# Performance work log

Measured on AMD Instinct MI355X. Metric: run time of the kernel, lower is better.

The kernel has to match this reference:

```python
import jax, jax.numpy as jnp
import numpy as np

B, S, D, H, F = 64, 512, 1024, 1024, 1024  # note: module requires H == D
EPS = 1e-6


def setup_inputs() -> dict:
    key = jax.random.key(0)
    ks = jax.random.split(key, 14)
    p = lambda k, shape: 0.02 * jax.random.normal(k, shape, dtype=jnp.float32)
    return {
        "hidden_state": jax.random.normal(ks[0], (B, S, D), dtype=jnp.float32),
        "field_hidden_state": jax.random.normal(ks[1], (B, S, F), dtype=jnp.float32),
        "input": jax.random.normal(ks[2], (B, D), dtype=jnp.float32),
        "finished": jnp.zeros((B, 1), dtype=bool),
        "W1": p(ks[3], (H, D)), "b1": p(ks[4], (H,)),
        "W2": p(ks[5], (H, D)), "b2": p(ks[6], (H,)),
        "W3": p(ks[7], (H, 2 * D)), "b3": p(ks[8], (H,)),
        "W4": p(ks[9], (H, F)), "b4": p(ks[10], (H,)),
        "W5": p(ks[11], (H, D)), "b5": p(ks[12], (H,)),
    }


def _norm_over_seq(w):
    # manual exp/max/sum softmax over seq dim (axis 0) with 1e-6 guard, as in torch
    w = jnp.exp(w - jnp.max(w, axis=0, keepdims=True))
    return w / (EPS + jnp.sum(w, axis=0, keepdims=True))


def reference(hidden_state, field_hidden_state, input, finished,
              W1, b1, W2, b2, W3, b3, W4, b4, W5, b5):
    hs = jnp.transpose(hidden_state, (1, 0, 2))        # [S, B, D]
    fs = jnp.transpose(field_hidden_state, (1, 0, 2))  # [S, B, F]
    phi_h = jnp.tanh(hs @ W1.T + b1)                   # [S, B, H]
    phi_f = jnp.tanh(fs @ W4.T + b4)                   # [S, B, H]

    gamma_h = jnp.tanh(input @ W2.T + b2)              # [B, H]
    weights = _norm_over_seq(jnp.sum(phi_h * gamma_h, axis=2, keepdims=True))  # [S, B, 1]

    alpha_h = jnp.tanh(input @ W5.T + b5)              # [B, H]
    field_w = _norm_over_seq(jnp.sum(phi_f * alpha_h, axis=2, keepdims=True))  # [S, B, 1]

    wf = weights * field_w
    weights = wf / (EPS + jnp.sum(wf, axis=0, keepdims=True))  # [S, B, 1]

    context = jnp.sum(hs * weights, axis=0)            # [B, D]
    out = jnp.concatenate([context, input], axis=-1) @ W3.T + b3  # [B, H]
    out = jnp.where(finished, jnp.zeros_like(out), out)
    return out, weights
```

## Files before the change

### kernel.cpp

```cpp
#include <hip/hip_runtime.h>

#define EPS 1e-6f

typedef _Float16 f16;
typedef _Float16 f16x8 __attribute__((ext_vector_type(8)));
typedef _Float16 f16x4 __attribute__((ext_vector_type(4)));
typedef float f32x4 __attribute__((ext_vector_type(4)));

__device__ __forceinline__ float tanh_fast(float x) {
    float e = __expf(2.0f * x);
    return 1.0f - 2.0f / (e + 1.0f);
}

__global__ __launch_bounds__(256) void wconv_kernel(
    const float* __restrict__ W1, const float* __restrict__ W4,
    f16* __restrict__ W1h, f16* __restrict__ W4h)
{
    int gid = blockIdx.x * 256 + threadIdx.x;
    const float4* s1 = (const float4*)W1;
    const float4* s4 = (const float4*)W4;
    f16x4* d1 = (f16x4*)W1h;
    f16x4* d4 = (f16x4*)W4h;
    #pragma unroll
    for (int r = 0; r < 2; ++r) {
        int i = gid + r * 131072;
        float4 v = s1[i];
        f16x4 o; o[0]=(f16)v.x; o[1]=(f16)v.y; o[2]=(f16)v.z; o[3]=(f16)v.w;
        d1[i] = o;
        float4 u = s4[i];
        f16x4 p; p[0]=(f16)u.x; p[1]=(f16)u.y; p[2]=(f16)u.z; p[3]=(f16)u.w;
        d4[i] = p;
    }
}

__global__ __launch_bounds__(256) void gamal_kernel(
    const float* __restrict__ inp,
    const float* __restrict__ W2, const float* __restrict__ b2,
    const float* __restrict__ W5, const float* __restrict__ b5,
    float* __restrict__ gamm, float* __restrict__ alph)
{
    const float* W  = blockIdx.y ? W5 : W2;
    const float* bs = blockIdx.y ? b5 : b2;
    float* dst      = blockIdx.y ? alph : gamm;
    int wid = threadIdx.x >> 6, lane = threadIdx.x & 63;
    int p = blockIdx.x * 4 + wid;
    int b = p >> 10, h = p & 1023;
    const float4* wr = (const float4*)(W + (size_t)h * 1024);
    const float4* xr = (const float4*)(inp + (size_t)b * 1024);
    float acc = 0.f;
    #pragma unroll
    for (int j = 0; j < 4; ++j) {
        float4 w4 = wr[lane + 64 * j];
        float4 x4 = xr[lane + 64 * j];
        acc += w4.x * x4.x + w4.y * x4.y + w4.z * x4.z + w4.w * x4.w;
    }
    #pragma unroll
    for (int o = 32; o; o >>= 1) acc += __shfl_xor(acc, o);
    if (lane == 0) dst[p] = tanh_fast(acc + bs[h]);
}

__global__ __launch_bounds__(256, 2) void fused_logits_kernel(
    const float* __restrict__ Ahid, const float* __restrict__ Afld,
    const f16* __restrict__ W1h, const f16* __restrict__ W4h,
    const float* __restrict__ b1, const float* __restrict__ b4,
    const float* __restrict__ gamm, const float* __restrict__ alph,
    float* __restrict__ Lh, float* __restrict__ Lf)
{
    const int mat = blockIdx.y;
    const float* A  = mat ? Afld : Ahid;
    const f16* W    = mat ? W4h : W1h;
    const float* bv = mat ? b4 : b1;
    const float* gv = mat ? alph : gamm;
    float* Lg       = mat ? Lf : Lh;

    const int m0 = blockIdx.x << 7;
    const int bidx = m0 >> 9;
    const int t = threadIdx.x;
    const int lane = t & 63;
    const int wid = t >> 6;
    const int wr = wid >> 1, wc = wid & 1;

    __shared__ __align__(16) f16 aL[2][128 * 40];
    __shared__ __align__(16) f16 wL[2][256 * 40];
    __shared__ float rowpart[128][2];

    if (t < 128) { rowpart[t][0] = 0.0f; rowpart[t][1] = 0.0f; }

    const int arow = t >> 1, ahalf = t & 1;
    const float* aG = A + (size_t)(m0 + arow) * 1024 + ahalf * 16;
    f16* aD0 = &aL[0][arow * 40 + ahalf * 16];
    f16* aD1 = &aL[1][arow * 40 + ahalf * 16];
    f16* wD0 = &wL[0][t * 40];
    f16* wD1 = &wL[1][t * 40];

    const int c16 = lane & 15;
    const int rq = lane >> 4;
    const int ks = rq << 3;
    const int rbase = (wr << 6) + c16;
    const int wbase = (wc << 7) + c16;

    f32x4 acc[4][8];

    for (int nc = 0; nc < 4; ++nc) {
        const f16* wG = W + (size_t)((nc << 8) + t) * 1024;
        f32x4 zz = {0.f, 0.f, 0.f, 0.f};
        #pragma unroll
        for (int mi = 0; mi < 4; ++mi)
            #pragma unroll
            for (int ni = 0; ni < 8; ++ni) acc[mi][ni] = zz;

        auto stage = [&](int kk, int buf) {
            const float4* ap = (const float4*)(aG + kk * 32);
            float4 x0 = ap[0], x1 = ap[1], x2 = ap[2], x3 = ap[3];
            const f16x8* wp = (const f16x8*)(wG + kk * 32);
            f16x8 w0 = wp[0], w1 = wp[1], w2 = wp[2], w3 = wp[3];
            f16x8 p0, p1;
            p0[0]=(f16)x0.x; p0[1]=(f16)x0.y; p0[2]=(f16)x0.z; p0[3]=(f16)x0.w;
            p0[4]=(f16)x1.x; p0[5]=(f16)x1.y; p0[6]=(f16)x1.z; p0[7]=(f16)x1.w;
            p1[0]=(f16)x2.x; p1[1]=(f16)x2.y; p1[2]=(f16)x2.z; p1[3]=(f16)x2.w;
            p1[4]=(f16)x3.x; p1[5]=(f16)x3.y; p1[6]=(f16)x3.z; p1[7]=(f16)x3.w;
            f16* ad = buf ? aD1 : aD0;
            f16* wd = buf ? wD1 : wD0;
            *(f16x8*)(ad)      = p0;
            *(f16x8*)(ad + 8)  = p1;
            *(f16x8*)(wd)      = w0;
            *(f16x8*)(wd + 8)  = w1;
            *(f16x8*)(wd + 16) = w2;
            *(f16x8*)(wd + 24) = w3;
        };

        stage(0, 0);
        __syncthreads();

        for (int kk = 0; kk < 32; ++kk) {
            const int cur = kk & 1;
            if (kk < 31) stage(kk + 1, cur ^ 1);
            const f16* aB = aL[cur];
            const f16* wB = wL[cur];
            f16x8 af[4];
            #pragma unroll
            for (int mi = 0; mi < 4; ++mi)
                af[mi] = *(const f16x8*)&aB[(rbase + mi * 16) * 40 + ks];
            #pragma unroll
            for (int ni = 0; ni < 8; ++ni) {
                f16x8 bf = *(const f16x8*)&wB[(wbase + ni * 16) * 40 + ks];
                #pragma unroll
                for (int mi = 0; mi < 4; ++mi)
                    acc[mi][ni] = __builtin_amdgcn_mfma_f32_16x16x32_f16(af[mi], bf, acc[mi][ni], 0, 0, 0);
            }
            __syncthreads();
        }

        float g[8], bb[8];
        #pragma unroll
        for (int ni = 0; ni < 8; ++ni) {
            int h = (nc << 8) + (wc << 7) + ni * 16 + c16;
            g[ni]  = gv[(bidx << 10) + h];
            bb[ni] = bv[h];
        }
        #pragma unroll
        for (int mi = 0; mi < 4; ++mi) {
            float v0 = 0.f, v1 = 0.f, v2 = 0.f, v3 = 0.f;
            #pragma unroll
            for (int ni = 0; ni < 8; ++ni) {
                v0 += tanh_fast(acc[mi][ni][0] + bb[ni]) * g[ni];
                v1 += tanh_fast(acc[mi][ni][1] + bb[ni]) * g[ni];
                v2 += tanh_fast(acc[mi][ni][2] + bb[ni]) * g[ni];
                v3 += tanh_fast(acc[mi][ni][3] + bb[ni]) * g[ni];
            }
            #pragma unroll
            for (int off = 1; off < 16; off <<= 1) {
                v0 += __shfl_xor(v0, off);
                v1 += __shfl_xor(v1, off);
                v2 += __shfl_xor(v2, off);
                v3 += __shfl_xor(v3, off);
            }
            if (c16 == 0) {
                int rb = (wr << 6) + mi * 16 + (rq << 2);
                rowpart[rb + 0][wc] += v0;
                rowpart[rb + 1][wc] += v1;
                rowpart[rb + 2][wc] += v2;
                rowpart[rb + 3][wc] += v3;
            }
        }
    }
    __syncthreads();
    if (t < 128) Lg[m0 + t] = rowpart[t][0] + rowpart[t][1];
}

__device__ __forceinline__ float blockMax(float v, float* sm) {
    #pragma unroll
    for (int o = 32; o; o >>= 1) v = fmaxf(v, __shfl_xor(v, o));
    if ((threadIdx.x & 63) == 0) sm[threadIdx.x >> 6] = v;
    __syncthreads();
    v = fmaxf(fmaxf(sm[0], sm[1]), fmaxf(sm[2], sm[3]));
    __syncthreads();
    return v;
}
__device__ __forceinline__ float blockSum(float v, float* sm) {
    #pragma unroll
    for (int o = 32; o; o >>= 1) v += __shfl_xor(v, o);
    if ((threadIdx.x & 63) == 0) sm[threadIdx.x >> 6] = v;
    __syncthreads();
    v = sm[0] + sm[1] + sm[2] + sm[3];
    __syncthreads();
    return v;
}

__global__ __launch_bounds__(256) void softmax_combine_kernel(
    const float* __restrict__ Lh, const float* __restrict__ Lf,
    float* __restrict__ wfin, float* __restrict__ dout)
{
    __shared__ float sm[4];
    int b = blockIdx.x, t = threadIdx.x;
    float h0 = Lh[b * 512 + t], h1 = Lh[b * 512 + 256 + t];
    float f0 = Lf[b * 512 + t], f1 = Lf[b * 512 + 256 + t];
    float mh = blockMax(fmaxf(h0, h1), sm);
    float mf = blockMax(fmaxf(f0, f1), sm);
    float e0 = __expf(h0 - mh), e1 = __expf(h1 - mh);
    float q0 = __expf(f0 - mf), q1 = __expf(f1 - mf);
    float sh = blockSum(e0 + e1, sm);
    float sf = blockSum(q0 + q1, sm);
    float wh0 = e0 / (EPS + sh), wh1 = e1 / (EPS + sh);
    float wq0 = q0 / (EPS + sf), wq1 = q1 / (EPS + sf);
    float c0 = wh0 * wq0, c1 = wh1 * wq1;
    float sc = blockSum(c0 + c1, sm);
    float r0 = c0 / (EPS + sc), r1 = c1 / (EPS + sc);
    wfin[b * 512 + t]       = r0;
    wfin[b * 512 + 256 + t] = r1;
    dout[65536 + t * 64 + b]         = r0;
    dout[65536 + (256 + t) * 64 + b] = r1;
}

__global__ __launch_bounds__(256) void context_kernel(
    const float* __restrict__ hs, const float* __restrict__ wgt,
    float* __restrict__ ctxpart)
{
    int dq = blockIdx.x;
    int b  = blockIdx.y;
    int sh = blockIdx.z;
    int t = threadIdx.x;
    int ss = t >> 6, ds = t & 63;
    __shared__ float4 part[4][64];
    const float4* hp = (const float4*)hs;
    float ax = 0.f, ay = 0.f, az = 0.f, aw = 0.f;
    int sBase = sh * 256 + ss * 64;
    for (int i = 0; i < 64; ++i) {
        int s = sBase + i;
        float w = wgt[b * 512 + s];
        float4 v = hp[(size_t)(b * 512 + s) * 256 + dq * 64 + ds];
        ax += v.x * w; ay += v.y * w; az += v.z * w; aw += v.w * w;
    }
    float4 r; r.x = ax; r.y = ay; r.z = az; r.w = aw;
    part[ss][ds] = r;
    __syncthreads();
    if (ss == 0) {
        float4 a0 = part[0][ds], a1 = part[1][ds], a2 = part[2][ds], a3 = part[3][ds];
        float4 o;
        o.x = a0.x + a1.x + a2.x + a3.x;
        o.y = a0.y + a1.y + a2.y + a3.y;
        o.z = a0.z + a1.z + a2.z + a3.z;
        o.w = a0.w + a1.w + a2.w + a3.w;
        ((float4*)ctxpart)[(size_t)sh * 16384 + b * 256 + dq * 64 + ds] = o;
    }
}

__global__ __launch_bounds__(256) void out_kernel(
    const float* __restrict__ ctxpart, const float* __restrict__ inp,
    const float* __restrict__ W3, const float* __restrict__ b3,
    const unsigned char* __restrict__ fin, float* __restrict__ out)
{
    int t = threadIdx.x, wid = t >> 6, lane = t & 63;
    int h = blockIdx.x * 4 + wid;
    __shared__ __align__(16) float xs[2048];
    float4* xsv = (float4*)xs;
    float4 wreg[8];
    const float4* w3r = (const float4*)(W3 + (size_t)h * 2048);
    #pragma unroll
    for (int j = 0; j < 8; ++j) wreg[j] = w3r[lane + 64 * j];
    const float4* cp = (const float4*)ctxpart;
    const float4* xp = (const float4*)inp;
    for (int b = 0; b < 64; ++b) {
        __syncthreads();
        {
            float4 c0 = cp[b * 256 + t];
            float4 c1 = cp[16384 + b * 256 + t];
            float4 cc; cc.x = c0.x + c1.x; cc.y = c0.y + c1.y;
            cc.z = c0.z + c1.z; cc.w = c0.w + c1.w;
            xsv[t] = cc;
            xsv[256 + t] = xp[b * 256 + t];
        }
        __syncthreads();
        float acc = 0.f;
        #pragma unroll
        for (int j = 0; j < 8; ++j) {
            float4 x = xsv[lane + 64 * j];
            acc += wreg[j].x * x.x + wreg[j].y * x.y + wreg[j].z * x.z + wreg[j].w * x.w;
        }
        #pragma unroll
        for (int o = 32; o; o >>= 1) acc += __shfl_xor(acc, o);
        if (lane == 0) out[b * 1024 + h] = fin[b] ? 0.f : (acc + b3[h]);
    }
}

extern "C" void kernel_launch(void* const* d_in, const int* in_sizes, int n_in,
                              void* d_out, int out_size, void* d_ws, size_t ws_size,
                              hipStream_t stream)
{
    const float* hidden = (const float*)d_in[0];
    const float* field  = (const float*)d_in[1];
    const float* input  = (const float*)d_in[2];
    const unsigned char* fin = (const unsigned char*)d_in[3];
    const float* W1 = (const float*)d_in[4];
    const float* b1 = (const float*)d_in[5];
    const float* W2 = (const float*)d_in[6];
    const float* b2 = (const float*)d_in[7];
    const float* W3 = (const float*)d_in[8];
    const float* b3 = (const float*)d_in[9];
    const float* W4 = (const float*)d_in[10];
    const float* b4 = (const float*)d_in[11];
    const float* W5 = (const float*)d_in[12];
    const float* b5 = (const float*)d_in[13];
    float* out = (float*)d_out;

    char* ws = (char*)d_ws;
    float* Lh   = (float*)(ws);
    float* Lf   = (float*)(ws + 131072);
    float* wfin = (float*)(ws + 262144);
    float* gamm = (float*)(ws + 393216);
    float* alph = (float*)(ws + 655360);
    float* ctxp = (float*)(ws + 917504);
    f16*   W1h  = (f16*)(ws + 1441792);
    f16*   W4h  = (f16*)(ws + 3538944);

    wconv_kernel<<<512, 256, 0, stream>>>(W1, W4, W1h, W4h);
    gamal_kernel<<<dim3(16384, 2), 256, 0, stream>>>(input, W2, b2, W5, b5, gamm, alph);
    fused_logits_kernel<<<dim3(256, 2), 256, 0, stream>>>(hidden, field, W1h, W4h,
                                                          b1, b4, gamm, alph, Lh, Lf);
    softmax_combine_kernel<<<64, 256, 0, stream>>>(Lh, Lf, wfin, out);
    context_kernel<<<dim3(4, 64, 2), 256, 0, stream>>>(hidden, wfin, ctxp);
    out_kernel<<<256, 256, 0, stream>>>(ctxp, input, W3, b3, fin, out);
}
```

Measured before the change: 369.7 us.

## Rewrite logits GEMM with 256x256 tiles, direct-to-LDS weight loads and N-split partials

The fused logits GEMM moves to 512-thread blocks, each computing a 256-row by 256-column tile with K steps of 64. The grid is split over the four hidden-column chunks, so each block writes partial row logits that the softmax kernel now sums. Weights go straight into LDS through global_load_lds with an XOR-swizzled layout, activations are prefetched two steps ahead and packed with cvt_pkrtz, and wave priority is raised around the MFMA bursts. The goal is higher MFMA utilisation, fewer LDS bank conflicts and more parallel blocks, at the cost of extra partial-logit traffic and heavier register and LDS use (128 KB of LDS per block).

```diff
diff --git a/kernel.cpp b/kernel.cpp
--- a/kernel.cpp
+++ b/kernel.cpp
@@ -3,8 +3,9 @@
 #define EPS 1e-6f
 
 typedef _Float16 f16;
+typedef __fp16 h16x2 __attribute__((ext_vector_type(2)));
+typedef _Float16 f16x4 __attribute__((ext_vector_type(4)));
 typedef _Float16 f16x8 __attribute__((ext_vector_type(8)));
-typedef _Float16 f16x4 __attribute__((ext_vector_type(4)));
 typedef float f32x4 __attribute__((ext_vector_type(4)));
 
 __device__ __forceinline__ float tanh_fast(float x) {
@@ -59,133 +60,182 @@
     if (lane == 0) dst[p] = tanh_fast(acc + bs[h]);
 }
 
-__global__ __launch_bounds__(256, 2) void fused_logits_kernel(
+__global__ __launch_bounds__(512, 2) void gemm_logits_kernel(
     const float* __restrict__ Ahid, const float* __restrict__ Afld,
     const f16* __restrict__ W1h, const f16* __restrict__ W4h,
     const float* __restrict__ b1, const float* __restrict__ b4,
     const float* __restrict__ gamm, const float* __restrict__ alph,
-    float* __restrict__ Lh, float* __restrict__ Lf)
-{
-    const int mat = blockIdx.y;
+    float* __restrict__ Lpart)
+{
+    __shared__ __align__(16) char smA[2][32768];
+    __shared__ __align__(16) char smW[2][32768];
+    __shared__ float rowpart[256][4];
+
+    const int lin = blockIdx.x;
+    const int swz = (lin & 7) * 128 + (lin >> 3);
+    const int mat = swz >> 9;
+    const int rem = swz & 511;
+    const int m_blk = rem >> 2;
+    const int nc = rem & 3;
+    const int m0 = m_blk << 8;
+    const int hc0 = nc << 8;
+
     const float* A  = mat ? Afld : Ahid;
-    const f16* W    = mat ? W4h : W1h;
+    const f16*  W   = mat ? W4h : W1h;
     const float* bv = mat ? b4 : b1;
     const float* gv = mat ? alph : gamm;
-    float* Lg       = mat ? Lf : Lh;
-
-    const int m0 = blockIdx.x << 7;
-    const int bidx = m0 >> 9;
+
     const int t = threadIdx.x;
     const int lane = t & 63;
-    const int wid = t >> 6;
-    const int wr = wid >> 1, wc = wid & 1;
-
-    __shared__ __align__(16) f16 aL[2][128 * 40];
-    __shared__ __align__(16) f16 wL[2][256 * 40];
-    __shared__ float rowpart[128][2];
-
-    if (t < 128) { rowpart[t][0] = 0.0f; rowpart[t][1] = 0.0f; }
-
-    const int arow = t >> 1, ahalf = t & 1;
-    const float* aG = A + (size_t)(m0 + arow) * 1024 + ahalf * 16;
-    f16* aD0 = &aL[0][arow * 40 + ahalf * 16];
-    f16* aD1 = &aL[1][arow * 40 + ahalf * 16];
-    f16* wD0 = &wL[0][t * 40];
-    f16* wD1 = &wL[1][t * 40];
-
+    const int wv = t >> 6;
+    const int wr = wv >> 2;
+    const int wc = wv & 3;
     const int c16 = lane & 15;
-    const int rq = lane >> 4;
-    const int ks = rq << 3;
-    const int rbase = (wr << 6) + c16;
-    const int wbase = (wc << 7) + c16;
-
-    f32x4 acc[4][8];
-
-    for (int nc = 0; nc < 4; ++nc) {
-        const f16* wG = W + (size_t)((nc << 8) + t) * 1024;
-        f32x4 zz = {0.f, 0.f, 0.f, 0.f};
-        #pragma unroll
-        for (int mi = 0; mi < 4; ++mi)
-            #pragma unroll
-            for (int ni = 0; ni < 8; ++ni) acc[mi][ni] = zz;
-
-        auto stage = [&](int kk, int buf) {
-            const float4* ap = (const float4*)(aG + kk * 32);
-            float4 x0 = ap[0], x1 = ap[1], x2 = ap[2], x3 = ap[3];
-            const f16x8* wp = (const f16x8*)(wG + kk * 32);
-            f16x8 w0 = wp[0], w1 = wp[1], w2 = wp[2], w3 = wp[3];
-            f16x8 p0, p1;
-            p0[0]=(f16)x0.x; p0[1]=(f16)x0.y; p0[2]=(f16)x0.z; p0[3]=(f16)x0.w;
-            p0[4]=(f16)x1.x; p0[5]=(f16)x1.y; p0[6]=(f16)x1.z; p0[7]=(f16)x1.w;
-            p1[0]=(f16)x2.x; p1[1]=(f16)x2.y; p1[2]=(f16)x2.z; p1[3]=(f16)x2.w;
-            p1[4]=(f16)x3.x; p1[5]=(f16)x3.y; p1[6]=(f16)x3.z; p1[7]=(f16)x3.w;
-            f16* ad = buf ? aD1 : aD0;
-            f16* wd = buf ? wD1 : wD0;
-            *(f16x8*)(ad)      = p0;
-            *(f16x8*)(ad + 8)  = p1;
-            *(f16x8*)(wd)      = w0;
-            *(f16x8*)(wd + 8)  = w1;
-            *(f16x8*)(wd + 16) = w2;
-            *(f16x8*)(wd + 24) = w3;
-        };
-
-        stage(0, 0);
-        __syncthreads();
-
-        for (int kk = 0; kk < 32; ++kk) {
-            const int cur = kk & 1;
-            if (kk < 31) stage(kk + 1, cur ^ 1);
-            const f16* aB = aL[cur];
-            const f16* wB = wL[cur];
-            f16x8 af[4];
-            #pragma unroll
-            for (int mi = 0; mi < 4; ++mi)
-                af[mi] = *(const f16x8*)&aB[(rbase + mi * 16) * 40 + ks];
-            #pragma unroll
-            for (int ni = 0; ni < 8; ++ni) {
-                f16x8 bf = *(const f16x8*)&wB[(wbase + ni * 16) * 40 + ks];
+    const int kg = lane >> 4;
+
+    const int srow = t >> 1;
+    const int shalf = t & 1;
+    const float* aRow = A + (size_t)(m0 + srow) * 1024 + shalf * 32;
+
+    const int lrow = lane >> 3, lslot = lane & 7;
+    const int kchunk = lslot ^ lrow;
+
+    const int swzr = (c16 & 7) << 4;
+    const int aoffb = (wr * 128 + c16) * 128;
+    const int woffb = (wc * 64 + c16) * 128;
+    const int kg16 = kg * 16;
+
+    f32x4 acc[8][4];
+    #pragma unroll
+    for (int i = 0; i < 8; ++i)
+        #pragma unroll
+        for (int j = 0; j < 4; ++j) acc[i][j] = (f32x4){0.f, 0.f, 0.f, 0.f};
+
+    float4 a_ld[8];
+
+    auto loadA = [&](int kt) {
+        const float4* ap = (const float4*)(aRow + kt * 64);
+        #pragma unroll
+        for (int j = 0; j < 8; ++j) a_ld[j] = ap[j];
+    };
+    auto writeA = [&](char* buf) {
+        char* ad = buf + srow * 128;
+        const int swzw = (srow & 7) << 4;
+        const int wb = shalf * 64;
+        #pragma unroll
+        for (int j = 0; j < 4; ++j) {
+            union { f16x8 v; h16x2 h[4]; } u;
+            float4 x = a_ld[2 * j], y = a_ld[2 * j + 1];
+            u.h[0] = __builtin_amdgcn_cvt_pkrtz(x.x, x.y);
+            u.h[1] = __builtin_amdgcn_cvt_pkrtz(x.z, x.w);
+            u.h[2] = __builtin_amdgcn_cvt_pkrtz(y.x, y.y);
+            u.h[3] = __builtin_amdgcn_cvt_pkrtz(y.z, y.w);
+            *(f16x8*)(ad + ((wb + j * 16) ^ swzw)) = u.v;
+        }
+    };
+    auto gloadW = [&](int kt, char* buf) {
+        #pragma unroll
+        for (int j = 0; j < 4; ++j) {
+            int r = wv * 32 + j * 8;
+            const f16* src = W + (size_t)(hc0 + r + lrow) * 1024 + kt * 64 + kchunk * 8;
+            char* dst = buf + r * 128;
+            __builtin_amdgcn_global_load_lds(
+                (const __attribute__((address_space(1))) void*)src,
+                (__attribute__((address_space(3))) void*)dst, 16, 0, 0);
+        }
+    };
+
+    loadA(0);
+    gloadW(0, smW[0]);
+    writeA(smA[0]);
+    loadA(1);
+    asm volatile("s_waitcnt vmcnt(8) lgkmcnt(0)" ::: "memory");
+    __builtin_amdgcn_sched_barrier(0);
+    __builtin_amdgcn_s_barrier();
+    __builtin_amdgcn_sched_barrier(0);
+
+    int cur = 0;
+    for (int kt = 0; kt < 16; ++kt) {
+        const int ktn  = kt < 15 ? kt + 1 : 15;
+        const int ktnn = kt < 14 ? kt + 2 : 15;
+        char* aC = smA[cur];
+        char* wC = smW[cur];
+        char* aN = smA[cur ^ 1];
+        char* wN = smW[cur ^ 1];
+
+        gloadW(ktn, wN);
+
+        {
+            f16x8 af[8], wf[4];
+            const int ko = kg16 ^ swzr;
+            #pragma unroll
+            for (int mi = 0; mi < 8; ++mi) af[mi] = *(const f16x8*)(aC + aoffb + mi * 2048 + ko);
+            #pragma unroll
+            for (int ni = 0; ni < 4; ++ni) wf[ni] = *(const f16x8*)(wC + woffb + ni * 2048 + ko);
+            __builtin_amdgcn_s_setprio(1);
+            #pragma unroll
+            for (int ni = 0; ni < 4; ++ni)
                 #pragma unroll
-                for (int mi = 0; mi < 4; ++mi)
-                    acc[mi][ni] = __builtin_amdgcn_mfma_f32_16x16x32_f16(af[mi], bf, acc[mi][ni], 0, 0, 0);
-            }
-            __syncthreads();
-        }
-
-        float g[8], bb[8];
-        #pragma unroll
-        for (int ni = 0; ni < 8; ++ni) {
-            int h = (nc << 8) + (wc << 7) + ni * 16 + c16;
-            g[ni]  = gv[(bidx << 10) + h];
-            bb[ni] = bv[h];
-        }
-        #pragma unroll
-        for (int mi = 0; mi < 4; ++mi) {
-            float v0 = 0.f, v1 = 0.f, v2 = 0.f, v3 = 0.f;
-            #pragma unroll
-            for (int ni = 0; ni < 8; ++ni) {
-                v0 += tanh_fast(acc[mi][ni][0] + bb[ni]) * g[ni];
-                v1 += tanh_fast(acc[mi][ni][1] + bb[ni]) * g[ni];
-                v2 += tanh_fast(acc[mi][ni][2] + bb[ni]) * g[ni];
-                v3 += tanh_fast(acc[mi][ni][3] + bb[ni]) * g[ni];
-            }
-            #pragma unroll
-            for (int off = 1; off < 16; off <<= 1) {
-                v0 += __shfl_xor(v0, off);
-                v1 += __shfl_xor(v1, off);
-                v2 += __shfl_xor(v2, off);
-                v3 += __shfl_xor(v3, off);
-            }
-            if (c16 == 0) {
-                int rb = (wr << 6) + mi * 16 + (rq << 2);
-                rowpart[rb + 0][wc] += v0;
-                rowpart[rb + 1][wc] += v1;
-                rowpart[rb + 2][wc] += v2;
-                rowpart[rb + 3][wc] += v3;
-            }
-        }
-    }
-    __syncthreads();
-    if (t < 128) Lg[m0 + t] = rowpart[t][0] + rowpart[t][1];
+                for (int mi = 0; mi < 8; ++mi)
+                    acc[mi][ni] = __builtin_amdgcn_mfma_f32_16x16x32_f16(af[mi], wf[ni], acc[mi][ni], 0, 0, 0);
+            __builtin_amdgcn_s_setprio(0);
+        }
+
+        f16x8 af1[8], wf1[4];
+        {
+            const int ko = (64 + kg16) ^ swzr;
+            #pragma unroll
+            for (int mi = 0; mi < 8; ++mi) af1[mi] = *(const f16x8*)(aC + aoffb + mi * 2048 + ko);
+            #pragma unroll
+            for (int ni = 0; ni < 4; ++ni) wf1[ni] = *(const f16x8*)(wC + woffb + ni * 2048 + ko);
+        }
+
+        writeA(aN);
+        loadA(ktnn);
+
+        __builtin_amdgcn_s_setprio(1);
+        #pragma unroll
+        for (int ni = 0; ni < 4; ++ni)
+            #pragma unroll
+            for (int mi = 0; mi < 8; ++mi)
+                acc[mi][ni] = __builtin_amdgcn_mfma_f32_16x16x32_f16(af1[mi], wf1[ni], acc[mi][ni], 0, 0, 0);
+        __builtin_amdgcn_s_setprio(0);
+
+        asm volatile("s_waitcnt vmcnt(8) lgkmcnt(0)" ::: "memory");
+        __builtin_amdgcn_sched_barrier(0);
+        __builtin_amdgcn_s_barrier();
+        __builtin_amdgcn_sched_barrier(0);
+        cur ^= 1;
+    }
+
+    const int bidx = m_blk >> 1;
+    float g[4], bb[4];
+    #pragma unroll
+    for (int ni = 0; ni < 4; ++ni) {
+        int h = hc0 + wc * 64 + ni * 16 + c16;
+        g[ni]  = gv[(bidx << 10) + h];
+        bb[ni] = bv[h];
+    }
+    #pragma unroll
+    for (int mi = 0; mi < 8; ++mi) {
+        #pragma unroll
+        for (int q = 0; q < 4; ++q) {
+            float v = tanh_fast(acc[mi][0][q] + bb[0]) * g[0]
+                    + tanh_fast(acc[mi][1][q] + bb[1]) * g[1]
+                    + tanh_fast(acc[mi][2][q] + bb[2]) * g[2]
+                    + tanh_fast(acc[mi][3][q] + bb[3]) * g[3];
+            v += __shfl_xor(v, 1);
+            v += __shfl_xor(v, 2);
+            v += __shfl_xor(v, 4);
+            v += __shfl_xor(v, 8);
+            if (c16 == 0)
+                rowpart[wr * 128 + mi * 16 + kg * 4 + q][wc] = v;
+        }
+    }
+    __syncthreads();
+    if (t < 256)
+        Lpart[(size_t)(mat * 4 + nc) * 32768 + m0 + t] =
+            rowpart[t][0] + rowpart[t][1] + rowpart[t][2] + rowpart[t][3];
 }
 
 __device__ __forceinline__ float blockMax(float v, float* sm) {
@@ -208,13 +258,19 @@
 }
 
 __global__ __launch_bounds__(256) void softmax_combine_kernel(
-    const float* __restrict__ Lh, const float* __restrict__ Lf,
+    const float* __restrict__ Lp,
     float* __restrict__ wfin, float* __restrict__ dout)
 {
     __shared__ float sm[4];
     int b = blockIdx.x, t = threadIdx.x;
-    float h0 = Lh[b * 512 + t], h1 = Lh[b * 512 + 256 + t];
-    float f0 = Lf[b * 512 + t], f1 = Lf[b * 512 + 256 + t];
+    float h0 = 0.f, h1 = 0.f, f0 = 0.f, f1 = 0.f;
+    #pragma unroll
+    for (int nc = 0; nc < 4; ++nc) {
+        h0 += Lp[nc * 32768 + b * 512 + t];
+        h1 += Lp[nc * 32768 + b * 512 + 256 + t];
+        f0 += Lp[(4 + nc) * 32768 + b * 512 + t];
+        f1 += Lp[(4 + nc) * 32768 + b * 512 + 256 + t];
+    }
     float mh = blockMax(fmaxf(h0, h1), sm);
     float mf = blockMax(fmaxf(f0, f1), sm);
     float e0 = __expf(h0 - mh), e1 = __expf(h1 - mh);
@@ -324,20 +380,19 @@
     float* out = (float*)d_out;
 
     char* ws = (char*)d_ws;
-    float* Lh   = (float*)(ws);
-    float* Lf   = (float*)(ws + 131072);
-    float* wfin = (float*)(ws + 262144);
-    float* gamm = (float*)(ws + 393216);
-    float* alph = (float*)(ws + 655360);
-    float* ctxp = (float*)(ws + 917504);
-    f16*   W1h  = (f16*)(ws + 1441792);
-    f16*   W4h  = (f16*)(ws + 3538944);
+    float* Lpart = (float*)(ws);
+    float* wfin  = (float*)(ws + 1048576);
+    float* gamm  = (float*)(ws + 1179648);
+    float* alph  = (float*)(ws + 1441792);
+    float* ctxp  = (float*)(ws + 1703936);
+    f16*   W1h   = (f16*)(ws + 2228224);
+    f16*   W4h   = (f16*)(ws + 4325376);
 
     wconv_kernel<<<512, 256, 0, stream>>>(W1, W4, W1h, W4h);
     gamal_kernel<<<dim3(16384, 2), 256, 0, stream>>>(input, W2, b2, W5, b5, gamm, alph);
-    fused_logits_kernel<<<dim3(256, 2), 256, 0, stream>>>(hidden, field, W1h, W4h,
-                                                          b1, b4, gamm, alph, Lh, Lf);
-    softmax_combine_kernel<<<64, 256, 0, stream>>>(Lh, Lf, wfin, out);
+    gemm_logits_kernel<<<1024, 512, 0, stream>>>(hidden, field, W1h, W4h,
+                                                 b1, b4, gamm, alph, Lpart);
+    softmax_combine_kernel<<<64, 256, 0, stream>>>(Lpart, wfin, out);
     context_kernel<<<dim3(4, 64, 2), 256, 0, stream>>>(hidden, wfin, ctxp);
     out_kernel<<<256, 256, 0, stream>>>(ctxp, input, W3, b3, fin, out);
 }
```

Result: slower. 382.7 us (+3.5%).
